# Performance work log

Hardware: AMD Instinct MI355X
Metric: run time of the kernel (lower is better)

The kernel has to match this reference:

```python
import jax, jax.numpy as jnp
import numpy as np
from jax import lax

LBDA = 0.5   # soft-min temperature from OTAM_cum_dist_v2 default
EPS = 0.01   # cos_sim epsilon


def otam_cum_dist(dists, lbda=LBDA):
    """Soft-DTW-style OTAM DP. dists: [nq, ns, L, S] -> [nq, ns].
    Faithful to OTAM_cum_dist_v2: pad last dim by (1,1) with zeros, then run the
    row-wise recurrence. Soft-min computed via stable logsumexp (same math as
    -lbda*log(sum exp(-x/lbda)))."""
    nq, ns, L, S = dists.shape
    d = jnp.pad(dists, ((0, 0), (0, 0), (0, 0), (1, 1)))  # [nq, ns, L, W], W=S+2
    W = S + 2
    # Row 0: cum[0, m] = cum[0, m-1] + d[0, m], cum[0, 0] = 0
    row0 = jnp.concatenate(
        [jnp.zeros((nq, ns, 1), d.dtype), jnp.cumsum(d[:, :, 0, 1:], axis=-1)], axis=-1)
    if L == 1:
        return row0[..., -1]

    m_idx = jnp.arange(1, W)
    include_up = (m_idx == 1) | (m_idx == W - 1)  # only first/last cols use cum[l-1, m]
    INF = jnp.asarray(jnp.inf, d.dtype)

    def row_step(prev_row, d_row):
        # prev_row, d_row: [nq, ns, W]
        xs = (
            jnp.moveaxis(d_row[:, :, 1:], -1, 0),        # d[l, m],       [W-1, nq, ns]
            jnp.moveaxis(prev_row[:, :, :-1], -1, 0),    # cum[l-1, m-1]
            jnp.moveaxis(prev_row[:, :, 1:], -1, 0),     # cum[l-1, m]
            include_up,
        )

        def col_step(cur_left, x):
            d_m, p_diag, p_up, inc = x
            up = jnp.where(inc, p_up, INF)               # masked term -> exp(-inf)=0
            terms = jnp.stack([p_diag, cur_left, up])    # [3, nq, ns]
            new = d_m - lbda * jax.nn.logsumexp(-terms / lbda, axis=0)
            return new, new

        _, cols = lax.scan(col_step, jnp.zeros((nq, ns), d.dtype), xs)
        row = jnp.concatenate(
            [jnp.zeros((nq, ns, 1), d.dtype), jnp.moveaxis(cols, 0, -1)], axis=-1)
        return row, None

    d_rows = jnp.moveaxis(d[:, :, 1:, :], 2, 0)          # [L-1, nq, ns, W]
    final_row, _ = lax.scan(row_step, row0, d_rows)
    return final_row[..., -1]


def reference(support_features, query_features):
    """OTAM meta-logits (cum_dist_g = -otam_distance) of DSN_TEMPORAL.
    support_features: [n_classes, L, D] class prototypes; query_features: [nq, L, D]."""
    nq, Lq, D = query_features.shape
    ns, Ls, _ = support_features.shape
    q = query_features.reshape(nq * Lq, D)
    s = support_features.reshape(ns * Ls, D)
    # cos_sim with epsilon in denominator (faithful to cos_sim())
    num = q @ s.T
    den = (jnp.linalg.norm(q, axis=-1)[:, None]
           * jnp.linalg.norm(s, axis=-1)[None, :] + EPS)
    frame_dists = 1.0 - num / den                         # [nq*L, ns*S]
    dists = frame_dists.reshape(nq, Lq, ns, Ls).transpose(0, 2, 1, 3)  # [nq, ns, L, S]
    cum = otam_cum_dist(dists) + otam_cum_dist(dists.transpose(0, 1, 3, 2))
    return -cum                                           # meta_logits [nq, ns]


def setup_inputs() -> dict:
    key = jax.random.key(0)
    k1, k2 = jax.random.split(key)
    return {
        "support_features": jax.random.normal(k1, (64, 8, 576), dtype=jnp.float32),
        "query_features": jax.random.normal(k2, (2048, 8, 576), dtype=jnp.float32),
    }
```

## Files before the change

kernel.cpp:

```cpp
#include <hip/hip_runtime.h>

#define D_K 576
#define NSLAB 18
#define LBDA_INV 2.0f
#define HALF_LBDA 0.5f
#define EPS 0.01f
#define DSTRIDE 136

#define NQROW 16384
#define NSROW 512
#define NQT 128
#define NST 4
#define NT 132
#define TILE_ELEMS (128 * D_K)
#define SLAB_ELEMS (128 * 32)

typedef __attribute__((ext_vector_type(8))) short short8;
typedef __attribute__((ext_vector_type(4))) short short4v;
typedef __attribute__((ext_vector_type(4))) float f32x4;

__device__ inline short f2bf(float f) {
    unsigned u = __float_as_uint(f);
    u += 0x7FFF + ((u >> 16) & 1);
    return (short)(u >> 16);
}
__device__ inline float bf2f(unsigned short s) {
    return __uint_as_float(((unsigned)s) << 16);
}

__global__ __launch_bounds__(256) void prep_kernel(
        const float* __restrict__ sup, const float* __restrict__ qry,
        unsigned short* __restrict__ tb, float* __restrict__ psum) {
    __shared__ unsigned short Ls[SLAB_ELEMS];
    const int t = threadIdx.x;
    const int slab = blockIdx.x;
    const int tile = blockIdx.y;
    const bool isq = tile < NQT;
    const float* src = (isq ? qry + (size_t)tile * 128 * D_K
                            : sup + (size_t)(tile - NQT) * 128 * D_K) + slab * 32;
    float* ps = psum + ((size_t)tile * NSLAB + slab) * 128;

#pragma unroll
    for (int i = 0; i < 4; ++i) {
        int idx = i * 256 + t;
        int r = idx >> 3, c = idx & 7;
        float4 v = *(const float4*)(src + (size_t)r * D_K + c * 4);
        float ss = v.x * v.x + v.y * v.y + v.z * v.z + v.w * v.w;
        ss += __shfl_down(ss, 4);
        ss += __shfl_down(ss, 2);
        ss += __shfl_down(ss, 1);
        if ((t & 7) == 0) ps[r] = ss;
        int c_in = c >> 1, half = c & 1;
        short4v o = {f2bf(v.x), f2bf(v.y), f2bf(v.z), f2bf(v.w)};
        *(short4v*)(&Ls[(c_in * 128 + r) * 8 + half * 4]) = o;
    }
    __syncthreads();
    unsigned short* dst = tb + (size_t)tile * TILE_ELEMS + (size_t)slab * SLAB_ELEMS;
    *(short8*)(dst + t * 16) = *(const short8*)(&Ls[t * 16]);
    *(short8*)(dst + t * 16 + 8) = *(const short8*)(&Ls[t * 16 + 8]);
}

__device__ inline float softmin3(float a, float b, float c) {
    float mn = fminf(a, fminf(b, c));
    float s = __expf(-LBDA_INV * (a - mn)) + __expf(-LBDA_INV * (b - mn)) +
              __expf(-LBDA_INV * (c - mn));
    return mn - HALF_LBDA * __logf(s);
}
__device__ inline float softmin2(float a, float b) {
    float mn = fminf(a, b);
    float s = __expf(-LBDA_INV * (a - mn)) + __expf(-LBDA_INV * (b - mn));
    return mn - HALF_LBDA * __logf(s);
}

template <int RS, int CS>
__device__ float otam_dp(const float* d) {
    float prev[10], cur[10];
    prev[0] = 0.f;
#pragma unroll
    for (int m = 1; m <= 8; ++m) prev[m] = prev[m - 1] + d[0 * RS + (m - 1) * CS];
    prev[9] = prev[8];
#pragma unroll
    for (int l = 1; l < 8; ++l) {
        cur[0] = 0.f;
        cur[1] = d[l * RS + 0 * CS] + softmin3(prev[0], 0.f, prev[1]);
#pragma unroll
        for (int m = 2; m <= 8; ++m)
            cur[m] = d[l * RS + (m - 1) * CS] + softmin2(prev[m - 1], cur[m - 1]);
        cur[9] = softmin3(prev[8], cur[8], prev[9]);
#pragma unroll
        for (int m = 0; m < 10; ++m) prev[m] = cur[m];
    }
    return prev[9];
}

__global__ __launch_bounds__(256, 2) void fused_kernel(
        const unsigned short* __restrict__ tb, const float* __restrict__ psum,
        float* __restrict__ out) {
    __shared__ unsigned short Ds[128 * DSTRIDE];
    __shared__ float qn_l[128], sn_l[128];

    const int t = threadIdx.x;
    const int b = blockIdx.x;
    const int xcd = b & 7, s2 = b >> 3;
    const int sblk = s2 >> 4;
    const int qblk = xcd * 16 + (s2 & 15);

    {
        const float* pq = psum + (size_t)qblk * NSLAB * 128;
        const float* ps = psum + (size_t)(NQT + sblk) * NSLAB * 128;
        if (t < 128) {
            float a = 0.f;
#pragma unroll
            for (int sl = 0; sl < NSLAB; ++sl) a += pq[sl * 128 + t];
            qn_l[t] = sqrtf(a);
        } else {
            int r = t - 128;
            float a = 0.f;
#pragma unroll
            for (int sl = 0; sl < NSLAB; ++sl) a += ps[sl * 128 + r];
            sn_l[r] = sqrtf(a);
        }
    }

    const unsigned short* At = tb + (size_t)qblk * TILE_ELEMS;
    const unsigned short* Bt = tb + (size_t)(NQT + sblk) * TILE_ELEMS;

    const int lane = t & 63;
    const int wave = t >> 6;
    const int wm = wave >> 1, wn = wave & 1;
    const int col16 = lane & 15, quad = lane >> 4;

    f32x4 acc[4][4];
#pragma unroll
    for (int i = 0; i < 4; ++i)
#pragma unroll
        for (int j = 0; j < 4; ++j) acc[i][j] = (f32x4){0.f, 0.f, 0.f, 0.f};

    int aoff[4], boff[4];
#pragma unroll
    for (int mt = 0; mt < 4; ++mt)
        aoff[mt] = (quad * 128 + wm * 64 + mt * 16 + col16) * 8;
#pragma unroll
    for (int nt = 0; nt < 4; ++nt)
        boff[nt] = (quad * 128 + wn * 64 + nt * 16 + col16) * 8;

#pragma unroll 3
    for (int sl = 0; sl < NSLAB; ++sl) {
        const unsigned short* Asl = At + sl * SLAB_ELEMS;
        const unsigned short* Bsl = Bt + sl * SLAB_ELEMS;
        short8 af[4], bf[4];
#pragma unroll
        for (int mt = 0; mt < 4; ++mt) af[mt] = *(const short8*)(Asl + aoff[mt]);
#pragma unroll
        for (int nt = 0; nt < 4; ++nt) bf[nt] = *(const short8*)(Bsl + boff[nt]);
#pragma unroll
        for (int mt = 0; mt < 4; ++mt)
#pragma unroll
            for (int nt = 0; nt < 4; ++nt)
                acc[mt][nt] = __builtin_amdgcn_mfma_f32_16x16x32_bf16(
                    af[mt], bf[nt], acc[mt][nt], 0, 0, 0);
    }
    __syncthreads();

#pragma unroll
    for (int mt = 0; mt < 4; ++mt) {
#pragma unroll
        for (int reg = 0; reg < 4; ++reg) {
            int m = wm * 64 + mt * 16 + quad * 4 + reg;
            float qv = qn_l[m];
#pragma unroll
            for (int nt = 0; nt < 4; ++nt) {
                int n = wn * 64 + nt * 16 + col16;
                float sv = sn_l[n];
                float dist = 1.f - acc[mt][nt][reg] / (qv * sv + EPS);
                Ds[m * DSTRIDE + n] = (unsigned short)f2bf(dist);
            }
        }
    }
    __syncthreads();

    const int ql = t >> 4, sl = t & 15;
    float d[64];
#pragma unroll
    for (int l = 0; l < 8; ++l) {
        short8 rowv = *(const short8*)(&Ds[(ql * 8 + l) * DSTRIDE + sl * 8]);
#pragma unroll
        for (int j = 0; j < 8; ++j) d[l * 8 + j] = bf2f((unsigned short)rowv[j]);
    }
    float r1 = otam_dp<8, 1>(d);
    float r2 = otam_dp<1, 8>(d);
    int qg = qblk * 16 + ql, sg = sblk * 16 + sl;
    out[qg * 64 + sg] = -(r1 + r2);
}

extern "C" void kernel_launch(void* const* d_in, const int* in_sizes, int n_in,
                              void* d_out, int out_size, void* d_ws, size_t ws_size,
                              hipStream_t stream) {
    const float* sup = (const float*)d_in[0];
    const float* qry = (const float*)d_in[1];
    float* out = (float*)d_out;

    unsigned short* tb = (unsigned short*)d_ws;
    float* psum = (float*)(tb + (size_t)NT * TILE_ELEMS);

    prep_kernel<<<dim3(NSLAB, NT), dim3(256), 0, stream>>>(sup, qry, tb, psum);
    fused_kernel<<<dim3(512), dim3(256), 0, stream>>>(tb, psum, out);
}
```

Measured before the change: 110.7 us.

## Fuse prep and GEMM-DP kernels into one persistent kernel with grid barrier

Merges the bf16 conversion/norm prep kernel into the main kernel. Each of 512 blocks handles a strided share of prep jobs, then all blocks meet at an atomic-counter grid barrier before the GEMM and DP stage. The goal is to remove one kernel launch and the gap between launches. In exchange it adds a memset launch, a spin barrier that assumes all 512 blocks are resident at once, and cross-block visibility that relies on threadfence.

```diff
diff --git a/kernel.cpp b/kernel.cpp
--- a/kernel.cpp
+++ b/kernel.cpp
@@ -14,6 +14,8 @@
 #define NT 132
 #define TILE_ELEMS (128 * D_K)
 #define SLAB_ELEMS (128 * 32)
+#define NJOBS (NT * NSLAB)
+#define NBLK 512
 
 typedef __attribute__((ext_vector_type(8))) short short8;
 typedef __attribute__((ext_vector_type(4))) short short4v;
@@ -26,38 +28,6 @@
 }
 __device__ inline float bf2f(unsigned short s) {
     return __uint_as_float(((unsigned)s) << 16);
-}
-
-__global__ __launch_bounds__(256) void prep_kernel(
-        const float* __restrict__ sup, const float* __restrict__ qry,
-        unsigned short* __restrict__ tb, float* __restrict__ psum) {
-    __shared__ unsigned short Ls[SLAB_ELEMS];
-    const int t = threadIdx.x;
-    const int slab = blockIdx.x;
-    const int tile = blockIdx.y;
-    const bool isq = tile < NQT;
-    const float* src = (isq ? qry + (size_t)tile * 128 * D_K
-                            : sup + (size_t)(tile - NQT) * 128 * D_K) + slab * 32;
-    float* ps = psum + ((size_t)tile * NSLAB + slab) * 128;
-
-#pragma unroll
-    for (int i = 0; i < 4; ++i) {
-        int idx = i * 256 + t;
-        int r = idx >> 3, c = idx & 7;
-        float4 v = *(const float4*)(src + (size_t)r * D_K + c * 4);
-        float ss = v.x * v.x + v.y * v.y + v.z * v.z + v.w * v.w;
-        ss += __shfl_down(ss, 4);
-        ss += __shfl_down(ss, 2);
-        ss += __shfl_down(ss, 1);
-        if ((t & 7) == 0) ps[r] = ss;
-        int c_in = c >> 1, half = c & 1;
-        short4v o = {f2bf(v.x), f2bf(v.y), f2bf(v.z), f2bf(v.w)};
-        *(short4v*)(&Ls[(c_in * 128 + r) * 8 + half * 4]) = o;
-    }
-    __syncthreads();
-    unsigned short* dst = tb + (size_t)tile * TILE_ELEMS + (size_t)slab * SLAB_ELEMS;
-    *(short8*)(dst + t * 16) = *(const short8*)(&Ls[t * 16]);
-    *(short8*)(dst + t * 16 + 8) = *(const short8*)(&Ls[t * 16 + 8]);
 }
 
 __device__ inline float softmin3(float a, float b, float c) {
@@ -93,14 +63,54 @@
     return prev[9];
 }
 
-__global__ __launch_bounds__(256, 2) void fused_kernel(
-        const unsigned short* __restrict__ tb, const float* __restrict__ psum,
-        float* __restrict__ out) {
+__global__ __launch_bounds__(256, 2) void mega_kernel(
+        const float* __restrict__ sup, const float* __restrict__ qry,
+        unsigned short* __restrict__ tb, float* __restrict__ psum,
+        unsigned* __restrict__ cnt, float* __restrict__ out) {
     __shared__ unsigned short Ds[128 * DSTRIDE];
     __shared__ float qn_l[128], sn_l[128];
 
     const int t = threadIdx.x;
     const int b = blockIdx.x;
+
+    int parity = 0;
+    for (int j = b; j < NJOBS; j += NBLK, parity ^= 1) {
+        unsigned short* Ls = Ds + parity * SLAB_ELEMS;
+        int tile = j / NSLAB;
+        int slab = j - tile * NSLAB;
+        const bool isq = tile < NQT;
+        const float* src = (isq ? qry + (size_t)tile * 128 * D_K
+                                : sup + (size_t)(tile - NQT) * 128 * D_K) + slab * 32;
+        float* ps = psum + ((size_t)tile * NSLAB + slab) * 128;
+#pragma unroll
+        for (int i = 0; i < 4; ++i) {
+            int idx = i * 256 + t;
+            int r = idx >> 3, c = idx & 7;
+            float4 v = *(const float4*)(src + (size_t)r * D_K + c * 4);
+            float ss = v.x * v.x + v.y * v.y + v.z * v.z + v.w * v.w;
+            ss += __shfl_down(ss, 4);
+            ss += __shfl_down(ss, 2);
+            ss += __shfl_down(ss, 1);
+            if ((t & 7) == 0) ps[r] = ss;
+            int c_in = c >> 1, half = c & 1;
+            short4v o = {f2bf(v.x), f2bf(v.y), f2bf(v.z), f2bf(v.w)};
+            *(short4v*)(&Ls[(c_in * 128 + r) * 8 + half * 4]) = o;
+        }
+        __syncthreads();
+        unsigned short* dst = tb + (size_t)tile * TILE_ELEMS + (size_t)slab * SLAB_ELEMS;
+        *(short8*)(dst + t * 16) = *(const short8*)(&Ls[t * 16]);
+        *(short8*)(dst + t * 16 + 8) = *(const short8*)(&Ls[t * 16 + 8]);
+    }
+
+    __syncthreads();
+    if (t == 0) {
+        __threadfence();
+        atomicAdd(cnt, 1u);
+        while (atomicAdd(cnt, 0u) < NBLK) __builtin_amdgcn_s_sleep(2);
+        __threadfence();
+    }
+    __syncthreads();
+
     const int xcd = b & 7, s2 = b >> 3;
     const int sblk = s2 >> 4;
     const int qblk = xcd * 16 + (s2 & 15);
@@ -202,7 +212,8 @@
 
     unsigned short* tb = (unsigned short*)d_ws;
     float* psum = (float*)(tb + (size_t)NT * TILE_ELEMS);
-
-    prep_kernel<<<dim3(NSLAB, NT), dim3(256), 0, stream>>>(sup, qry, tb, psum);
-    fused_kernel<<<dim3(512), dim3(256), 0, stream>>>(tb, psum, out);
-}
+    unsigned* cnt = (unsigned*)(psum + (size_t)NT * NSLAB * 128);
+
+    hipMemsetAsync(cnt, 0, sizeof(unsigned), stream);
+    mega_kernel<<<dim3(NBLK), dim3(256), 0, stream>>>(sup, qry, tb, psum, cnt, out);
+}
```

Measured after the change: 175.3 us. +58.4%, slower.

## Stage GEMM operand slabs through LDS with direct global-to-LDS loads

Applied to the files above, without the earlier changes.

Replaces per-wave direct global loads of A/B fragments with cooperative global_load_lds transfers of two K-slabs of each operand into shared memory, then reads MFMA fragments from LDS. This lets each tile byte be fetched once per block rather than redundantly by the waves sharing a row or column, and reuses the Ds buffer for staging. It adds two barriers per iteration with no double buffering, so load latency is exposed and not overlapped with MFMA work.

```diff
diff --git a/kernel.cpp b/kernel.cpp
--- a/kernel.cpp
+++ b/kernel.cpp
@@ -7,8 +7,6 @@
 #define EPS 0.01f
 #define DSTRIDE 136
 
-#define NQROW 16384
-#define NSROW 512
 #define NQT 128
 #define NST 4
 #define NT 132
@@ -26,6 +24,13 @@
 }
 __device__ inline float bf2f(unsigned short s) {
     return __uint_as_float(((unsigned)s) << 16);
+}
+
+__device__ inline void load_lds16(const void* g, void* l) {
+    __builtin_amdgcn_global_load_lds(
+        (const __attribute__((address_space(1))) unsigned int*)g,
+        (__attribute__((address_space(3))) unsigned int*)l,
+        16, 0, 0);
 }
 
 __global__ __launch_bounds__(256) void prep_kernel(
@@ -96,8 +101,13 @@
 __global__ __launch_bounds__(256, 2) void fused_kernel(
         const unsigned short* __restrict__ tb, const float* __restrict__ psum,
         float* __restrict__ out) {
-    __shared__ unsigned short Ds[128 * DSTRIDE];
+    __shared__ unsigned short smem[128 * DSTRIDE];
     __shared__ float qn_l[128], sn_l[128];
+    unsigned short* As0 = smem;
+    unsigned short* As1 = smem + SLAB_ELEMS;
+    unsigned short* Bs0 = smem + 2 * SLAB_ELEMS;
+    unsigned short* Bs1 = smem + 3 * SLAB_ELEMS;
+    unsigned short* Ds = smem;
 
     const int t = threadIdx.x;
     const int b = blockIdx.x;
@@ -105,21 +115,19 @@
     const int sblk = s2 >> 4;
     const int qblk = xcd * 16 + (s2 & 15);
 
-    {
+    if (t < 128) {
         const float* pq = psum + (size_t)qblk * NSLAB * 128;
+        float a = 0.f;
+#pragma unroll
+        for (int sl = 0; sl < NSLAB; ++sl) a += pq[sl * 128 + t];
+        qn_l[t] = sqrtf(a);
+    } else {
+        int r = t - 128;
         const float* ps = psum + (size_t)(NQT + sblk) * NSLAB * 128;
-        if (t < 128) {
-            float a = 0.f;
-#pragma unroll
-            for (int sl = 0; sl < NSLAB; ++sl) a += pq[sl * 128 + t];
-            qn_l[t] = sqrtf(a);
-        } else {
-            int r = t - 128;
-            float a = 0.f;
-#pragma unroll
-            for (int sl = 0; sl < NSLAB; ++sl) a += ps[sl * 128 + r];
-            sn_l[r] = sqrtf(a);
-        }
+        float a = 0.f;
+#pragma unroll
+        for (int sl = 0; sl < NSLAB; ++sl) a += ps[sl * 128 + r];
+        sn_l[r] = sqrtf(a);
     }
 
     const unsigned short* At = tb + (size_t)qblk * TILE_ELEMS;
@@ -144,23 +152,40 @@
     for (int nt = 0; nt < 4; ++nt)
         boff[nt] = (quad * 128 + wn * 64 + nt * 16 + col16) * 8;
 
-#pragma unroll 3
-    for (int sl = 0; sl < NSLAB; ++sl) {
-        const unsigned short* Asl = At + sl * SLAB_ELEMS;
-        const unsigned short* Bsl = Bt + sl * SLAB_ELEMS;
-        short8 af[4], bf[4];
-#pragma unroll
-        for (int mt = 0; mt < 4; ++mt) af[mt] = *(const short8*)(Asl + aoff[mt]);
-#pragma unroll
-        for (int nt = 0; nt < 4; ++nt) bf[nt] = *(const short8*)(Bsl + boff[nt]);
-#pragma unroll
-        for (int mt = 0; mt < 4; ++mt)
-#pragma unroll
-            for (int nt = 0; nt < 4; ++nt)
-                acc[mt][nt] = __builtin_amdgcn_mfma_f32_16x16x32_bf16(
-                    af[mt], bf[nt], acc[mt][nt], 0, 0, 0);
-    }
-    __syncthreads();
+    for (int j2 = 0; j2 < 9; ++j2) {
+        const unsigned short* A0 = At + (size_t)(2 * j2) * SLAB_ELEMS;
+        const unsigned short* A1 = A0 + SLAB_ELEMS;
+        const unsigned short* B0 = Bt + (size_t)(2 * j2) * SLAB_ELEMS;
+        const unsigned short* B1 = B0 + SLAB_ELEMS;
+#pragma unroll
+        for (int i = 0; i < 2; ++i) {
+            int cb = wave * 128 + i * 64;
+            int go = (cb + lane) * 8;
+            load_lds16(A0 + go, &As0[cb * 8]);
+            load_lds16(A1 + go, &As1[cb * 8]);
+            load_lds16(B0 + go, &Bs0[cb * 8]);
+            load_lds16(B1 + go, &Bs1[cb * 8]);
+        }
+        __syncthreads();
+
+#pragma unroll
+        for (int h = 0; h < 2; ++h) {
+            const unsigned short* Ah = h ? As1 : As0;
+            const unsigned short* Bh = h ? Bs1 : Bs0;
+            short8 af[4], bf[4];
+#pragma unroll
+            for (int mt = 0; mt < 4; ++mt) af[mt] = *(const short8*)(Ah + aoff[mt]);
+#pragma unroll
+            for (int nt = 0; nt < 4; ++nt) bf[nt] = *(const short8*)(Bh + boff[nt]);
+#pragma unroll
+            for (int mt = 0; mt < 4; ++mt)
+#pragma unroll
+                for (int nt = 0; nt < 4; ++nt)
+                    acc[mt][nt] = __builtin_amdgcn_mfma_f32_16x16x32_bf16(
+                        af[mt], bf[nt], acc[mt][nt], 0, 0, 0);
+        }
+        __syncthreads();
+    }
 
 #pragma unroll
     for (int mt = 0; mt < 4; ++mt) {
```

Measured after the change: 112.1 us. About the same (+1.3%).
